# Optimization experiments

Hardware: AMD Instinct MI355X
Metric: run time of the kernel (lower is better)

## Reference

```python
import jax, jax.numpy as jnp
import numpy as np

EMBED = 256      # embedding_dim
HEADS = 4        # attn_heads
OUT = EMBED // HEADS  # out_channels per head = 64
R = 8            # n_relations = len(metapaths) + 1
N = 16384        # num_nodes
NEG_SLOPE = 0.2  # PyG GATv2 default leaky_relu slope


def setup_inputs() -> dict:
    key = jax.random.key(0)
    ks = jax.random.split(key, 16)
    s = 0.05
    inp = {"relation_embs": jax.random.normal(ks[0], (N, R, EMBED), jnp.float32)}
    # Two GATv2Conv layers: lin_l (src), lin_r (dst), att vector, output bias.
    for i in range(2):
        inp[f"Wl{i}"] = jax.random.normal(ks[1 + 6 * i], (EMBED, HEADS, OUT), jnp.float32) * s
        inp[f"bl{i}"] = jax.random.normal(ks[2 + 6 * i], (HEADS, OUT), jnp.float32) * s
        inp[f"Wr{i}"] = jax.random.normal(ks[3 + 6 * i], (EMBED, HEADS, OUT), jnp.float32) * s
        inp[f"br{i}"] = jax.random.normal(ks[4 + 6 * i], (HEADS, OUT), jnp.float32) * s
        inp[f"att{i}"] = jax.random.normal(ks[5 + 6 * i], (HEADS, OUT), jnp.float32) * s
        inp[f"bias{i}"] = jax.random.normal(ks[6 + 6 * i], (HEADS * OUT,), jnp.float32) * s
    return inp


def reference(relation_embs, Wl0, bl0, Wr0, br0, att0, bias0,
              Wl1, bl1, Wr1, br1, att1, bias1):
    # Each node owns a fully-connected graph over its R relation embeddings
    # (all rows nonzero under randn fill), so the PyG gather/softmax/scatter
    # collapses to dense [N, R_dst, R_src] attention.
    h = jax.nn.relu(relation_embs)                                  # [N,R,D]

    # ---- GATv2 layer 0: full FC edges (every src -> every dst) ----
    xl = jnp.einsum('nrd,dhc->nrhc', h, Wl0) + bl0                  # src feats [N,R,H,C]
    xr = jnp.einsum('nrd,dhc->nrhc', h, Wr0) + br0                  # dst feats [N,R,H,C]
    e = jax.nn.leaky_relu(xr[:, :, None] + xl[:, None], NEG_SLOPE)  # [N,Ri,Rj,H,C]
    logits = jnp.einsum('nijhc,hc->nijh', e, att0)                  # [N,Ri,Rj,H]
    alpha = jax.nn.softmax(logits, axis=2)                          # softmax over src j
    h = jnp.einsum('nijh,njhc->nihc', alpha, xl)                    # [N,R,H,C]
    h = h.reshape(N, R, HEADS * OUT) + bias0
    h = jax.nn.relu(h)

    # ---- GATv2 layer 1 (last): only edges into the self node (nid == R-1) ----
    xl = jnp.einsum('nrd,dhc->nrhc', h, Wl1) + bl1                  # src feats [N,R,H,C]
    xr_self = jnp.einsum('nd,dhc->nhc', h[:, -1], Wr1) + br1        # dst = self [N,H,C]
    e = jax.nn.leaky_relu(xr_self[:, None] + xl, NEG_SLOPE)         # [N,R,H,C]
    logits = jnp.einsum('nrhc,hc->nrh', e, att1)                    # [N,R,H]
    alpha = jax.nn.softmax(logits, axis=1)                          # softmax over src r
    out = jnp.einsum('nrh,nrhc->nhc', alpha, xl).reshape(N, HEADS * OUT) + bias1
    node_embs = jax.nn.relu(out)                                    # [N, D]

    # betas: last-layer attention into the self node, detached (SparseTensor.to_dense().detach())
    betas = jax.lax.stop_gradient(alpha)                            # [N,R,H]
    return node_embs, betas
```

## Files before the change

### kernel.cpp

```cpp
#include <hip/hip_runtime.h>


#define NNODES 16384
#define NB 8
#define MR 64

typedef _Float16 f16x8 __attribute__((ext_vector_type(8)));
typedef _Float16 f16x4 __attribute__((ext_vector_type(4)));
typedef _Float16 f16x2 __attribute__((ext_vector_type(2)));
typedef float f32x4 __attribute__((ext_vector_type(4)));

#if __has_builtin(__builtin_amdgcn_fdot2)
#define FDOT2(a, b, c) __builtin_amdgcn_fdot2((a), (b), (c), false)
#else
#define FDOT2(a, b, c) ((c) + (float)(a)[0] * (float)(b)[0] + (float)(a)[1] * (float)(b)[1])
#endif

__device__ __forceinline__ f16x2 pk2(float a, float b) {
    return __builtin_bit_cast(f16x2, __builtin_amdgcn_cvt_pkrtz(a, b));
}

__device__ __forceinline__ f16x2 leaky2(f16x2 t) {
#if __has_builtin(__builtin_elementwise_max)
    return __builtin_elementwise_max(t, t * (f16x2){(_Float16)0.2f, (_Float16)0.2f});
#else
    const unsigned u = __builtin_bit_cast(unsigned, t) & 0x7FFF7FFFu;
    const f16x2 at = __builtin_bit_cast(f16x2, u);
    return t * (f16x2){(_Float16)0.6f, (_Float16)0.6f} +
           at * (f16x2){(_Float16)0.4f, (_Float16)0.4f};
#endif
}
__device__ __forceinline__ f16x2 relu2(f16x2 t) {
#if __has_builtin(__builtin_elementwise_max)
    return __builtin_elementwise_max(t, (f16x2){(_Float16)0.f, (_Float16)0.f});
#else
    const unsigned u = __builtin_bit_cast(unsigned, t) & 0x7FFF7FFFu;
    const f16x2 at = __builtin_bit_cast(f16x2, u);
    return (t + at) * (f16x2){(_Float16)0.5f, (_Float16)0.5f};
#endif
}

__device__ __forceinline__ int swz(int row, int chunk) {
    return row * 256 + ((chunk ^ (row & 7)) << 3);
}

__global__ void prep_weights(const float* __restrict__ Wl0, const float* __restrict__ Wr0,
                             const float* __restrict__ Wl1, const float* __restrict__ Wr1,
                             _Float16* __restrict__ wt) {
    __shared__ float tile[64 * 68];
    const int t  = threadIdx.x;
    const int m  = blockIdx.x >> 4;
    const int kt = (blockIdx.x >> 2) & 3;
    const int nt = blockIdx.x & 3;
    const float* src = (m == 0 ? Wl0 : m == 1 ? Wr0 : m == 2 ? Wl1 : Wr1) + kt * 64 * 256;
    #pragma unroll
    for (int i = 0; i < 4; ++i) {
        const int idx = i * 256 + t;
        const int kk  = idx >> 4;
        const int nn  = (idx & 15) * 4;
        const float4 v = *(const float4*)&src[kk * 256 + nt * 64 + nn];
        tile[kk * 68 + nn + 0] = v.x;
        tile[kk * 68 + nn + 1] = v.y;
        tile[kk * 68 + nn + 2] = v.z;
        tile[kk * 68 + nn + 3] = v.w;
    }
    __syncthreads();
    const int n  = t >> 2;
    const int ks = (t & 3) * 16;
    f16x8 o0, o1;
    #pragma unroll
    for (int e = 0; e < 8; ++e) o0[e] = (_Float16)tile[(ks + e) * 68 + n];
    #pragma unroll
    for (int e = 0; e < 8; ++e) o1[e] = (_Float16)tile[(ks + 8 + e) * 68 + n];
    _Float16* dst = &wt[(size_t)(m * 256 + nt * 64 + n) * 256 + kt * 64 + ks];
    *(f16x8*)dst = o0;
    *(f16x8*)(dst + 8) = o1;
}

__launch_bounds__(512, 4)
__global__ void gat_fused(const float* __restrict__ x,
                          const float* __restrict__ bl0, const float* __restrict__ br0,
                          const float* __restrict__ att0, const float* __restrict__ bias0,
                          const float* __restrict__ bl1, const float* __restrict__ br1,
                          const float* __restrict__ att1, const float* __restrict__ bias1,
                          const _Float16* __restrict__ wt,
                          float* __restrict__ out) {
    __shared__ _Float16 bufA[MR * 256];
    __shared__ _Float16 bufB[MR * 256];
    __shared__ float attbuf[2304];
    __shared__ _Float16 attH[768];

    const int tid  = threadIdx.x;
    const int bg   = blockIdx.x;
    const int lane = tid & 63;
    const int wv   = tid >> 6;
    const int lr   = lane & 15;
    const int lq   = lane >> 4;

    {
        const float4* src = (const float4*)(x + (size_t)bg * (MR * 256));
        #pragma unroll
        for (int it = 0; it < 4; ++it) {
            const int g   = it * 512 + tid;
            const int row = g >> 5;
            const int c   = g & 31;
            const float4 v0 = src[2 * g];
            const float4 v1 = src[2 * g + 1];
            f16x8 s;
            s[0] = (_Float16)fmaxf(v0.x, 0.f); s[1] = (_Float16)fmaxf(v0.y, 0.f);
            s[2] = (_Float16)fmaxf(v0.z, 0.f); s[3] = (_Float16)fmaxf(v0.w, 0.f);
            s[4] = (_Float16)fmaxf(v1.x, 0.f); s[5] = (_Float16)fmaxf(v1.y, 0.f);
            s[6] = (_Float16)fmaxf(v1.z, 0.f); s[7] = (_Float16)fmaxf(v1.w, 0.f);
            *(f16x8*)&bufA[swz(row, c)] = s;
        }
        if (tid < 256) {
            attH[tid]       = (_Float16)att0[tid];
            attH[512 + tid] = (_Float16)bias0[tid];
        } else {
            attH[tid]       = (_Float16)att1[tid - 256];
        }
    }
    __syncthreads();

    {
        f32x4 acc[4][4];
        #pragma unroll
        for (int m = 0; m < 4; ++m)
            #pragma unroll
            for (int n = 0; n < 4; ++n)
                acc[m][n] = f32x4{0.f, 0.f, 0.f, 0.f};
        #pragma unroll
        for (int kt = 0; kt < 8; ++kt) {
            f16x8 a[4], b[4];
            #pragma unroll
            for (int m = 0; m < 4; ++m)
                a[m] = *(const f16x8*)&bufA[swz(m * 16 + lr, kt * 4 + lq)];
            const int koff = kt * 32 + lq * 8;
            #pragma unroll
            for (int n = 0; n < 4; ++n)
                b[n] = *(const f16x8*)&wt[(size_t)(wv * 64 + n * 16 + lr) * 256 + koff];
            #pragma unroll
            for (int m = 0; m < 4; ++m)
                #pragma unroll
                for (int n = 0; n < 4; ++n)
                    acc[m][n] = __builtin_amdgcn_mfma_f32_16x16x32_f16(a[m], b[n], acc[m][n], 0, 0, 0);
        }
        __syncthreads();
        _Float16* dstbuf = (wv < 4) ? bufB : bufA;
        const float* bv = (wv < 4) ? bl0 : br0;
        #pragma unroll
        for (int n = 0; n < 4; ++n) {
            const int cl   = (wv & 3) * 64 + n * 16 + lr;
            const float bias = bv[cl];
            const int ch   = cl >> 3, ce = cl & 7;
            #pragma unroll
            for (int m = 0; m < 4; ++m)
                #pragma unroll
                for (int r = 0; r < 4; ++r) {
                    const int row = m * 16 + lq * 4 + r;
                    dstbuf[swz(row, ch) + ce] = (_Float16)(acc[m][n][r] + bias);
                }
        }
    }
    __syncthreads();

    {
        const int n  = tid >> 6;
        const int i  = (tid >> 3) & 7;
        const int h  = (tid >> 1) & 3;
        const int jh = tid & 1;
        const int rowR = n * 8 + i;
        f16x2 xr2[32];
        #pragma unroll
        for (int cc = 0; cc < 8; ++cc) {
            const int c3 = (cc + 2 * h) & 7;
            const f16x8 v = *(const f16x8*)&bufA[swz(rowR, h * 8 + c3)];
            xr2[cc * 4 + 0] = f16x2{v[0], v[1]};
            xr2[cc * 4 + 1] = f16x2{v[2], v[3]};
            xr2[cc * 4 + 2] = f16x2{v[4], v[5]};
            xr2[cc * 4 + 3] = f16x2{v[6], v[7]};
        }
        f16x8 lbuf[2][4];
        f16x8 abuf[2];
        {
            const int c3 = (2 * h) & 7;
            abuf[0] = *(const f16x8*)&attH[h * 64 + c3 * 8];
            #pragma unroll
            for (int jj = 0; jj < 4; ++jj)
                lbuf[0][jj] = *(const f16x8*)&bufB[swz(n * 8 + jh * 4 + jj, h * 8 + c3)];
        }
        float lg[4] = {0.f, 0.f, 0.f, 0.f};
        #pragma unroll
        for (int cc = 0; cc < 8; ++cc) {
            const int cur = cc & 1, nxt = cur ^ 1;
            if (cc < 7) {
                const int c3n = (cc + 1 + 2 * h) & 7;
                abuf[nxt] = *(const f16x8*)&attH[h * 64 + c3n * 8];
                #pragma unroll
                for (int jj = 0; jj < 4; ++jj)
                    lbuf[nxt][jj] = *(const f16x8*)&bufB[swz(n * 8 + jh * 4 + jj, h * 8 + c3n)];
            }
            const f16x8 a8 = abuf[cur];
            const f16x2 a2[4] = {{a8[0], a8[1]}, {a8[2], a8[3]}, {a8[4], a8[5]}, {a8[6], a8[7]}};
            #pragma unroll
            for (int jj = 0; jj < 4; ++jj) {
                const f16x8 l8 = lbuf[cur][jj];
                const f16x2 l2[4] = {{l8[0], l8[1]}, {l8[2], l8[3]}, {l8[4], l8[5]}, {l8[6], l8[7]}};
                #pragma unroll
                for (int p = 0; p < 4; ++p) {
                    const f16x2 t = leaky2(xr2[cc * 4 + p] + l2[p]);
                    lg[jj] = FDOT2(t, a2[p], lg[jj]);
                }
            }
        }
        float mx = fmaxf(fmaxf(lg[0], lg[1]), fmaxf(lg[2], lg[3]));
        mx = fmaxf(mx, __shfl_xor(mx, 1));
        float ex[4], ssum = 0.f;
        #pragma unroll
        for (int jj = 0; jj < 4; ++jj) { ex[jj] = __expf(lg[jj] - mx); ssum += ex[jj]; }
        const float tot = ssum + __shfl_xor(ssum, 1);
        const float inv = 1.f / tot;
        #pragma unroll
        for (int jj = 0; jj < 4; ++jj)
            attbuf[((n * 8 + i) * 4 + h) * 8 + jh * 4 + jj] = ex[jj] * inv;
    }
    __syncthreads();

    {
        const int row  = tid >> 3;
        const int sub  = tid & 7;
        const int h    = sub >> 1;
        const int half = sub & 1;
        const int nn   = row >> 3;
        const int cb   = h * 8 + half * 4;
        _Float16 ahv[8];
        #pragma unroll
        for (int j = 0; j < 8; ++j) ahv[j] = (_Float16)attbuf[(row * 4 + h) * 8 + j];
        f16x2 acc2[16];
        #pragma unroll
        for (int p = 0; p < 16; ++p) acc2[p] = (f16x2){(_Float16)0.f, (_Float16)0.f};
        f16x8 vbuf[2][4];
        #pragma unroll
        for (int cc = 0; cc < 4; ++cc)
            vbuf[0][cc] = *(const f16x8*)&bufB[swz(nn * 8, cb + ((cc + h) & 3))];
        #pragma unroll
        for (int j = 0; j < 8; ++j) {
            const int cur = j & 1, nxt = cur ^ 1;
            if (j < 7) {
                #pragma unroll
                for (int cc = 0; cc < 4; ++cc)
                    vbuf[nxt][cc] = *(const f16x8*)&bufB[swz(nn * 8 + j + 1, cb + ((cc + h) & 3))];
            }
            const f16x2 a2 = {ahv[j], ahv[j]};
            #pragma unroll
            for (int cc = 0; cc < 4; ++cc) {
                const f16x8 v = vbuf[cur][cc];
                acc2[cc * 4 + 0] += f16x2{v[0], v[1]} * a2;
                acc2[cc * 4 + 1] += f16x2{v[2], v[3]} * a2;
                acc2[cc * 4 + 2] += f16x2{v[4], v[5]} * a2;
                acc2[cc * 4 + 3] += f16x2{v[6], v[7]} * a2;
            }
        }
        #pragma unroll
        for (int cc = 0; cc < 4; ++cc) {
            const int c = cb + ((cc + h) & 3);
            const f16x8 b8 = *(const f16x8*)&attH[512 + c * 8];
            f16x8 s;
            #pragma unroll
            for (int p = 0; p < 4; ++p) {
                const f16x2 r = relu2(acc2[cc * 4 + p] + f16x2{b8[2 * p], b8[2 * p + 1]});
                s[2 * p]     = r[0];
                s[2 * p + 1] = r[1];
            }
            *(f16x8*)&bufA[swz(row, c)] = s;
        }
    }
    __syncthreads();

    {
        f32x4 accl[4][2], accr[2];
        #pragma unroll
        for (int m = 0; m < 4; ++m)
            #pragma unroll
            for (int n = 0; n < 2; ++n)
                accl[m][n] = f32x4{0.f, 0.f, 0.f, 0.f};
        #pragma unroll
        for (int n = 0; n < 2; ++n) accr[n] = f32x4{0.f, 0.f, 0.f, 0.f};
        const _Float16* W1l = wt + 512 * 256;
        const _Float16* W1r = wt + 768 * 256;
        const int rowS = (lr & 7) * 8 + 7;
        #pragma unroll
        for (int kt = 0; kt < 8; ++kt) {
            const int koff = kt * 32 + lq * 8;
            f16x8 a[4], as, bl[2], br[2];
            #pragma unroll
            for (int m = 0; m < 4; ++m)
                a[m] = *(const f16x8*)&bufA[swz(m * 16 + lr, kt * 4 + lq)];
            as = *(const f16x8*)&bufA[swz(rowS, kt * 4 + lq)];
            #pragma unroll
            for (int n = 0; n < 2; ++n) {
                bl[n] = *(const f16x8*)&W1l[(size_t)(wv * 32 + n * 16 + lr) * 256 + koff];
                br[n] = *(const f16x8*)&W1r[(size_t)(wv * 32 + n * 16 + lr) * 256 + koff];
            }
            #pragma unroll
            for (int m = 0; m < 4; ++m)
                #pragma unroll
                for (int n = 0; n < 2; ++n)
                    accl[m][n] = __builtin_amdgcn_mfma_f32_16x16x32_f16(a[m], bl[n], accl[m][n], 0, 0, 0);
            #pragma unroll
            for (int n = 0; n < 2; ++n)
                accr[n] = __builtin_amdgcn_mfma_f32_16x16x32_f16(as, br[n], accr[n], 0, 0, 0);
        }
        #pragma unroll
        for (int n = 0; n < 2; ++n) {
            const int col = wv * 32 + n * 16 + lr;
            const float b1 = bl1[col], b2 = br1[col];
            const int ch = col >> 3, ce = col & 7;
            #pragma unroll
            for (int m = 0; m < 4; ++m)
                #pragma unroll
                for (int r = 0; r < 4; ++r) {
                    const int row = m * 16 + lq * 4 + r;
                    bufB[swz(row, ch) + ce] = (_Float16)(accl[m][n][r] + b1);
                }
            if (lq < 2) {
                #pragma unroll
                for (int r = 0; r < 4; ++r) {
                    const int node = lq * 4 + r;
                    attbuf[node * 256 + col] = accr[n][r] + b2;
                }
            }
        }
    }
    __syncthreads();

    {
        const int n  = tid >> 5;
        const int rr = (tid >> 2) & 7;
        const int h  = tid & 3;
        float lg = 0.f;
        if (tid < 256) {
            const int rowj = n * 8 + rr;
            float4 xbuf0[2], xbuf1[2];
            f16x8 lbuf[2], abuf[2];
            {
                const int c = h * 8 + ((2 * h) & 7);
                xbuf0[0] = *(const float4*)&attbuf[n * 256 + c * 8];
                xbuf1[0] = *(const float4*)&attbuf[n * 256 + c * 8 + 4];
                lbuf[0]  = *(const f16x8*)&bufB[swz(rowj, c)];
                abuf[0]  = *(const f16x8*)&attH[256 + c * 8];
            }
            #pragma unroll
            for (int cc = 0; cc < 8; ++cc) {
                const int cur = cc & 1, nxt = cur ^ 1;
                if (cc < 7) {
                    const int cn = h * 8 + ((cc + 1 + 2 * h) & 7);
                    xbuf0[nxt] = *(const float4*)&attbuf[n * 256 + cn * 8];
                    xbuf1[nxt] = *(const float4*)&attbuf[n * 256 + cn * 8 + 4];
                    lbuf[nxt]  = *(const f16x8*)&bufB[swz(rowj, cn)];
                    abuf[nxt]  = *(const f16x8*)&attH[256 + cn * 8];
                }
                const float4 r0 = xbuf0[cur], r1 = xbuf1[cur];
                const f16x2 x2[4] = {pk2(r0.x, r0.y), pk2(r0.z, r0.w),
                                     pk2(r1.x, r1.y), pk2(r1.z, r1.w)};
                const f16x8 l8 = lbuf[cur];
                const f16x2 l2[4] = {{l8[0], l8[1]}, {l8[2], l8[3]}, {l8[4], l8[5]}, {l8[6], l8[7]}};
                const f16x8 a8 = abuf[cur];
                const f16x2 a2[4] = {{a8[0], a8[1]}, {a8[2], a8[3]}, {a8[4], a8[5]}, {a8[6], a8[7]}};
                #pragma unroll
                for (int p = 0; p < 4; ++p) {
                    const f16x2 t = leaky2(x2[p] + l2[p]);
                    lg = FDOT2(t, a2[p], lg);
                }
            }
        }
        __syncthreads();
        if (tid < 256) attbuf[2048 + tid] = lg;
        __syncthreads();
        if (tid < 256) {
            float M = -1e30f;
            float l[8];
            #pragma unroll
            for (int j = 0; j < 8; ++j) {
                l[j] = attbuf[2048 + n * 32 + j * 4 + h];
                M = fmaxf(M, l[j]);
            }
            float S = 0.f;
            #pragma unroll
            for (int j = 0; j < 8; ++j) S += __expf(l[j] - M);
            const float a = __expf(lg - M) / S;
            attbuf[tid] = a;
            out[(size_t)NNODES * 256 + (size_t)(bg * NB + n) * 32 + rr * 4 + h] = a;
        }
    }
    __syncthreads();

    {
        const int n  = tid >> 6;
        const int q  = tid & 63;
        const int c0 = q * 4;
        const int h  = q >> 4;
        f16x4 v[8];
        float a[8];
        #pragma unroll
        for (int r = 0; r < 8; ++r) {
            v[r] = *(const f16x4*)&bufB[swz(n * 8 + r, q >> 1) + (q & 1) * 4];
            a[r] = attbuf[n * 32 + r * 4 + h];
        }
        float o0 = 0.f, o1 = 0.f, o2 = 0.f, o3 = 0.f;
        #pragma unroll
        for (int r = 0; r < 8; ++r) {
            o0 = fmaf((float)v[r][0], a[r], o0);
            o1 = fmaf((float)v[r][1], a[r], o1);
            o2 = fmaf((float)v[r][2], a[r], o2);
            o3 = fmaf((float)v[r][3], a[r], o3);
        }
        float4 res;
        res.x = fmaxf(o0 + bias1[c0 + 0], 0.f);
        res.y = fmaxf(o1 + bias1[c0 + 1], 0.f);
        res.z = fmaxf(o2 + bias1[c0 + 2], 0.f);
        res.w = fmaxf(o3 + bias1[c0 + 3], 0.f);
        *(float4*)&out[(size_t)(bg * NB + n) * 256 + c0] = res;
    }
}

extern "C" void kernel_launch(void* const* d_in, const int* in_sizes, int n_in,
                              void* d_out, int out_size, void* d_ws, size_t ws_size,
                              hipStream_t stream) {
    const float* x     = (const float*)d_in[0];
    const float* Wl0   = (const float*)d_in[1];
    const float* bl0   = (const float*)d_in[2];
    const float* Wr0   = (const float*)d_in[3];
    const float* br0   = (const float*)d_in[4];
    const float* att0  = (const float*)d_in[5];
    const float* bias0 = (const float*)d_in[6];
    const float* Wl1   = (const float*)d_in[7];
    const float* bl1   = (const float*)d_in[8];
    const float* Wr1   = (const float*)d_in[9];
    const float* br1   = (const float*)d_in[10];
    const float* att1  = (const float*)d_in[11];
    const float* bias1 = (const float*)d_in[12];
    _Float16* wt = (_Float16*)d_ws;
    float* out = (float*)d_out;

    prep_weights<<<64, 256, 0, stream>>>(Wl0, Wr0, Wl1, Wr1, wt);
    gat_fused<<<NNODES / NB, 512, 0, stream>>>(x, bl0, br0, att0, bias0,
                                               bl1, br1, att1, bias1, wt, out);
}
```

Baseline: 350.7 us.

## Halve per-block node tile to 4 nodes with 256 threads and fp16 LDS buffers

Shrinks each block from 8 nodes/512 threads to 4 nodes/256 threads, remapping the MFMA warp tiling so each wave covers more output columns and fewer rows. The shared float attbuf is replaced by smaller fp16 buffers for attention weights and self-destination features, plus separate logit and alpha arrays, which removes a barrier and the float-to-half packing in layer 1. The aim is lower LDS per block so more blocks fit per CU, and better latency hiding. The cost is that each block now re-reads the full weight matrices for half as many nodes, doubling global and L2 weight traffic.

```diff
diff --git a/kernel.cpp b/kernel.cpp
--- a/kernel.cpp
+++ b/kernel.cpp
@@ -2,8 +2,8 @@
 
 
 #define NNODES 16384
-#define NB 8
-#define MR 64
+#define NB 4
+#define MR 32
 
 typedef _Float16 f16x8 __attribute__((ext_vector_type(8)));
 typedef _Float16 f16x4 __attribute__((ext_vector_type(4)));
@@ -15,10 +15,6 @@
 #else
 #define FDOT2(a, b, c) ((c) + (float)(a)[0] * (float)(b)[0] + (float)(a)[1] * (float)(b)[1])
 #endif
-
-__device__ __forceinline__ f16x2 pk2(float a, float b) {
-    return __builtin_bit_cast(f16x2, __builtin_amdgcn_cvt_pkrtz(a, b));
-}
 
 __device__ __forceinline__ f16x2 leaky2(f16x2 t) {
 #if __has_builtin(__builtin_elementwise_max)
@@ -77,7 +73,7 @@
     *(f16x8*)(dst + 8) = o1;
 }
 
-__launch_bounds__(512, 4)
+__launch_bounds__(256, 4)
 __global__ void gat_fused(const float* __restrict__ x,
                           const float* __restrict__ bl0, const float* __restrict__ br0,
                           const float* __restrict__ att0, const float* __restrict__ bias0,
@@ -87,7 +83,10 @@
                           float* __restrict__ out) {
     __shared__ _Float16 bufA[MR * 256];
     __shared__ _Float16 bufB[MR * 256];
-    __shared__ float attbuf[2304];
+    __shared__ _Float16 aw[MR * 4 * 8];
+    __shared__ _Float16 xrsH[NB * 256];
+    __shared__ float lgs[NB * 32];
+    __shared__ float al1[NB * 32];
     __shared__ _Float16 attH[768];
 
     const int tid  = threadIdx.x;
@@ -101,7 +100,7 @@
         const float4* src = (const float4*)(x + (size_t)bg * (MR * 256));
         #pragma unroll
         for (int it = 0; it < 4; ++it) {
-            const int g   = it * 512 + tid;
+            const int g   = it * 256 + tid;
             const int row = g >> 5;
             const int c   = g & 31;
             const float4 v0 = src[2 * g];
@@ -113,48 +112,45 @@
             s[6] = (_Float16)fmaxf(v1.z, 0.f); s[7] = (_Float16)fmaxf(v1.w, 0.f);
             *(f16x8*)&bufA[swz(row, c)] = s;
         }
-        if (tid < 256) {
-            attH[tid]       = (_Float16)att0[tid];
-            attH[512 + tid] = (_Float16)bias0[tid];
-        } else {
-            attH[tid]       = (_Float16)att1[tid - 256];
-        }
-    }
-    __syncthreads();
-
-    {
-        f32x4 acc[4][4];
-        #pragma unroll
-        for (int m = 0; m < 4; ++m)
-            #pragma unroll
-            for (int n = 0; n < 4; ++n)
+        attH[tid]       = (_Float16)att0[tid];
+        attH[256 + tid] = (_Float16)att1[tid];
+        attH[512 + tid] = (_Float16)bias0[tid];
+    }
+    __syncthreads();
+
+    {
+        f32x4 acc[2][8];
+        #pragma unroll
+        for (int m = 0; m < 2; ++m)
+            #pragma unroll
+            for (int n = 0; n < 8; ++n)
                 acc[m][n] = f32x4{0.f, 0.f, 0.f, 0.f};
         #pragma unroll
         for (int kt = 0; kt < 8; ++kt) {
-            f16x8 a[4], b[4];
-            #pragma unroll
-            for (int m = 0; m < 4; ++m)
+            f16x8 a[2], b[8];
+            #pragma unroll
+            for (int m = 0; m < 2; ++m)
                 a[m] = *(const f16x8*)&bufA[swz(m * 16 + lr, kt * 4 + lq)];
             const int koff = kt * 32 + lq * 8;
             #pragma unroll
-            for (int n = 0; n < 4; ++n)
-                b[n] = *(const f16x8*)&wt[(size_t)(wv * 64 + n * 16 + lr) * 256 + koff];
-            #pragma unroll
-            for (int m = 0; m < 4; ++m)
-                #pragma unroll
-                for (int n = 0; n < 4; ++n)
+            for (int n = 0; n < 8; ++n)
+                b[n] = *(const f16x8*)&wt[(size_t)(wv * 128 + n * 16 + lr) * 256 + koff];
+            #pragma unroll
+            for (int m = 0; m < 2; ++m)
+                #pragma unroll
+                for (int n = 0; n < 8; ++n)
                     acc[m][n] = __builtin_amdgcn_mfma_f32_16x16x32_f16(a[m], b[n], acc[m][n], 0, 0, 0);
         }
         __syncthreads();
-        _Float16* dstbuf = (wv < 4) ? bufB : bufA;
-        const float* bv = (wv < 4) ? bl0 : br0;
-        #pragma unroll
-        for (int n = 0; n < 4; ++n) {
-            const int cl   = (wv & 3) * 64 + n * 16 + lr;
+        _Float16* dstbuf = (wv < 2) ? bufB : bufA;
+        const float* bv = (wv < 2) ? bl0 : br0;
+        #pragma unroll
+        for (int n = 0; n < 8; ++n) {
+            const int cl   = (wv & 1) * 128 + n * 16 + lr;
             const float bias = bv[cl];
             const int ch   = cl >> 3, ce = cl & 7;
             #pragma unroll
-            for (int m = 0; m < 4; ++m)
+            for (int m = 0; m < 2; ++m)
                 #pragma unroll
                 for (int r = 0; r < 4; ++r) {
                     const int row = m * 16 + lq * 4 + r;
@@ -220,9 +216,10 @@
         for (int jj = 0; jj < 4; ++jj) { ex[jj] = __expf(lg[jj] - mx); ssum += ex[jj]; }
         const float tot = ssum + __shfl_xor(ssum, 1);
         const float inv = 1.f / tot;
-        #pragma unroll
-        for (int jj = 0; jj < 4; ++jj)
-            attbuf[((n * 8 + i) * 4 + h) * 8 + jh * 4 + jj] = ex[jj] * inv;
+        f16x4 w;
+        #pragma unroll
+        for (int jj = 0; jj < 4; ++jj) w[jj] = (_Float16)(ex[jj] * inv);
+        *(f16x4*)&aw[((n * 8 + i) * 4 + h) * 8 + jh * 4] = w;
     }
     __syncthreads();
 
@@ -233,9 +230,7 @@
         const int half = sub & 1;
         const int nn   = row >> 3;
         const int cb   = h * 8 + half * 4;
-        _Float16 ahv[8];
-        #pragma unroll
-        for (int j = 0; j < 8; ++j) ahv[j] = (_Float16)attbuf[(row * 4 + h) * 8 + j];
+        const f16x8 ah8 = *(const f16x8*)&aw[(row * 4 + h) * 8];
         f16x2 acc2[16];
         #pragma unroll
         for (int p = 0; p < 16; ++p) acc2[p] = (f16x2){(_Float16)0.f, (_Float16)0.f};
@@ -251,7 +246,7 @@
                 for (int cc = 0; cc < 4; ++cc)
                     vbuf[nxt][cc] = *(const f16x8*)&bufB[swz(nn * 8 + j + 1, cb + ((cc + h) & 3))];
             }
-            const f16x2 a2 = {ahv[j], ahv[j]};
+            const f16x2 a2 = {ah8[j], ah8[j]};
             #pragma unroll
             for (int cc = 0; cc < 4; ++cc) {
                 const f16x8 v = vbuf[cur][cc];
@@ -278,57 +273,55 @@
     __syncthreads();
 
     {
-        f32x4 accl[4][2], accr[2];
-        #pragma unroll
-        for (int m = 0; m < 4; ++m)
-            #pragma unroll
-            for (int n = 0; n < 2; ++n)
+        f32x4 accl[2][4], accr[4];
+        #pragma unroll
+        for (int m = 0; m < 2; ++m)
+            #pragma unroll
+            for (int n = 0; n < 4; ++n)
                 accl[m][n] = f32x4{0.f, 0.f, 0.f, 0.f};
         #pragma unroll
-        for (int n = 0; n < 2; ++n) accr[n] = f32x4{0.f, 0.f, 0.f, 0.f};
+        for (int n = 0; n < 4; ++n) accr[n] = f32x4{0.f, 0.f, 0.f, 0.f};
         const _Float16* W1l = wt + 512 * 256;
         const _Float16* W1r = wt + 768 * 256;
-        const int rowS = (lr & 7) * 8 + 7;
+        const int rowS = (lr & 3) * 8 + 7;
         #pragma unroll
         for (int kt = 0; kt < 8; ++kt) {
             const int koff = kt * 32 + lq * 8;
-            f16x8 a[4], as, bl[2], br[2];
-            #pragma unroll
-            for (int m = 0; m < 4; ++m)
+            f16x8 a[2], as, bl[4], br[4];
+            #pragma unroll
+            for (int m = 0; m < 2; ++m)
                 a[m] = *(const f16x8*)&bufA[swz(m * 16 + lr, kt * 4 + lq)];
             as = *(const f16x8*)&bufA[swz(rowS, kt * 4 + lq)];
             #pragma unroll
-            for (int n = 0; n < 2; ++n) {
-                bl[n] = *(const f16x8*)&W1l[(size_t)(wv * 32 + n * 16 + lr) * 256 + koff];
-                br[n] = *(const f16x8*)&W1r[(size_t)(wv * 32 + n * 16 + lr) * 256 + koff];
-            }
-            #pragma unroll
-            for (int m = 0; m < 4; ++m)
-                #pragma unroll
-                for (int n = 0; n < 2; ++n)
+            for (int n = 0; n < 4; ++n) {
+                bl[n] = *(const f16x8*)&W1l[(size_t)(wv * 64 + n * 16 + lr) * 256 + koff];
+                br[n] = *(const f16x8*)&W1r[(size_t)(wv * 64 + n * 16 + lr) * 256 + koff];
+            }
+            #pragma unroll
+            for (int m = 0; m < 2; ++m)
+                #pragma unroll
+                for (int n = 0; n < 4; ++n)
                     accl[m][n] = __builtin_amdgcn_mfma_f32_16x16x32_f16(a[m], bl[n], accl[m][n], 0, 0, 0);
             #pragma unroll
-            for (int n = 0; n < 2; ++n)
+            for (int n = 0; n < 4; ++n)
                 accr[n] = __builtin_amdgcn_mfma_f32_16x16x32_f16(as, br[n], accr[n], 0, 0, 0);
         }
         #pragma unroll
-        for (int n = 0; n < 2; ++n) {
-            const int col = wv * 32 + n * 16 + lr;
+        for (int n = 0; n < 4; ++n) {
+            const int col = wv * 64 + n * 16 + lr;
             const float b1 = bl1[col], b2 = br1[col];
             const int ch = col >> 3, ce = col & 7;
             #pragma unroll
-            for (int m = 0; m < 4; ++m)
+            for (int m = 0; m < 2; ++m)
                 #pragma unroll
                 for (int r = 0; r < 4; ++r) {
                     const int row = m * 16 + lq * 4 + r;
                     bufB[swz(row, ch) + ce] = (_Float16)(accl[m][n][r] + b1);
                 }
-            if (lq < 2) {
-                #pragma unroll
-                for (int r = 0; r < 4; ++r) {
-                    const int node = lq * 4 + r;
-                    attbuf[node * 256 + col] = accr[n][r] + b2;
-                }
+            if (lq == 0) {
+                #pragma unroll
+                for (int r = 0; r < 4; ++r)
+                    xrsH[r * 256 + col] = (_Float16)(accr[n][r] + b2);
             }
         }
     }
@@ -339,57 +332,52 @@
         const int rr = (tid >> 2) & 7;
         const int h  = tid & 3;
         float lg = 0.f;
-        if (tid < 256) {
+        if (tid < 128) {
             const int rowj = n * 8 + rr;
-            float4 xbuf0[2], xbuf1[2];
-            f16x8 lbuf[2], abuf[2];
+            f16x8 xbuf[2], lbuf[2], abuf[2];
             {
                 const int c = h * 8 + ((2 * h) & 7);
-                xbuf0[0] = *(const float4*)&attbuf[n * 256 + c * 8];
-                xbuf1[0] = *(const float4*)&attbuf[n * 256 + c * 8 + 4];
-                lbuf[0]  = *(const f16x8*)&bufB[swz(rowj, c)];
-                abuf[0]  = *(const f16x8*)&attH[256 + c * 8];
+                xbuf[0] = *(const f16x8*)&xrsH[n * 256 + c * 8];
+                lbuf[0] = *(const f16x8*)&bufB[swz(rowj, c)];
+                abuf[0] = *(const f16x8*)&attH[256 + c * 8];
             }
             #pragma unroll
             for (int cc = 0; cc < 8; ++cc) {
                 const int cur = cc & 1, nxt = cur ^ 1;
                 if (cc < 7) {
                     const int cn = h * 8 + ((cc + 1 + 2 * h) & 7);
-                    xbuf0[nxt] = *(const float4*)&attbuf[n * 256 + cn * 8];
-                    xbuf1[nxt] = *(const float4*)&attbuf[n * 256 + cn * 8 + 4];
-                    lbuf[nxt]  = *(const f16x8*)&bufB[swz(rowj, cn)];
-                    abuf[nxt]  = *(const f16x8*)&attH[256 + cn * 8];
+                    xbuf[nxt] = *(const f16x8*)&xrsH[n * 256 + cn * 8];
+                    lbuf[nxt] = *(const f16x8*)&bufB[swz(rowj, cn)];
+                    abuf[nxt] = *(const f16x8*)&attH[256 + cn * 8];
                 }
-                const float4 r0 = xbuf0[cur], r1 = xbuf1[cur];
-                const f16x2 x2[4] = {pk2(r0.x, r0.y), pk2(r0.z, r0.w),
-                                     pk2(r1.x, r1.y), pk2(r1.z, r1.w)};
+                const f16x8 x8 = xbuf[cur];
                 const f16x8 l8 = lbuf[cur];
-                const f16x2 l2[4] = {{l8[0], l8[1]}, {l8[2], l8[3]}, {l8[4], l8[5]}, {l8[6], l8[7]}};
                 const f16x8 a8 = abuf[cur];
-                const f16x2 a2[4] = {{a8[0], a8[1]}, {a8[2], a8[3]}, {a8[4], a8[5]}, {a8[6], a8[7]}};
                 #pragma unroll
                 for (int p = 0; p < 4; ++p) {
-                    const f16x2 t = leaky2(x2[p] + l2[p]);
-                    lg = FDOT2(t, a2[p], lg);
+                    const f16x2 xp = {x8[2 * p], x8[2 * p + 1]};
+                    const f16x2 lp = {l8[2 * p], l8[2 * p + 1]};
+                    const f16x2 ap = {a8[2 * p], a8[2 * p + 1]};
+                    const f16x2 t = leaky2(xp + lp);
+                    lg = FDOT2(t, ap, lg);
                 }
             }
+            lgs[tid] = lg;
         }
         __syncthreads();
-        if (tid < 256) attbuf[2048 + tid] = lg;
-        __syncthreads();
-        if (tid < 256) {
+        if (tid < 128) {
             float M = -1e30f;
             float l[8];
             #pragma unroll
             for (int j = 0; j < 8; ++j) {
-                l[j] = attbuf[2048 + n * 32 + j * 4 + h];
+                l[j] = lgs[n * 32 + j * 4 + h];
                 M = fmaxf(M, l[j]);
             }
             float S = 0.f;
             #pragma unroll
             for (int j = 0; j < 8; ++j) S += __expf(l[j] - M);
             const float a = __expf(lg - M) / S;
-            attbuf[tid] = a;
+            al1[tid] = a;
             out[(size_t)NNODES * 256 + (size_t)(bg * NB + n) * 32 + rr * 4 + h] = a;
         }
     }
@@ -405,7 +393,7 @@
         #pragma unroll
         for (int r = 0; r < 8; ++r) {
             v[r] = *(const f16x4*)&bufB[swz(n * 8 + r, q >> 1) + (q & 1) * 4];
-            a[r] = attbuf[n * 32 + r * 4 + h];
+            a[r] = al1[n * 32 + r * 4 + h];
         }
         float o0 = 0.f, o1 = 0.f, o2 = 0.f, o3 = 0.f;
         #pragma unroll
@@ -444,6 +432,6 @@
     float* out = (float*)d_out;
 
     prep_weights<<<64, 256, 0, stream>>>(Wl0, Wr0, Wl1, Wr1, wt);
-    gat_fused<<<NNODES / NB, 512, 0, stream>>>(x, bl0, br0, att0, bias0,
+    gat_fused<<<NNODES / NB, 256, 0, stream>>>(x, bl0, br0, att0, bias0,
                                                bl1, br1, att1, bias1, wt, out);
 }
```

Result: slower. 432.2 us (+23.2%).

## Split layer-0 projection GEMM into separate kernel with fp16 workspace intermediate

Applied to the files above, without the earlier changes.

Splits the fused kernel in two. A standalone GEMM kernel over 128-row tiles computes the layer-0 src/dst projections and writes them as fp16 into a workspace buffer. A second kernel reads that buffer and does the attention, the layer-1 GEMM and the output. This gives the first GEMM larger tiles and better weight reuse, at the cost of an extra global round trip of about 128MB (written, then read back) and a larger workspace requirement. If the workspace is too small, it falls back to the original fused kernel.

```diff
diff --git a/kernel.cpp b/kernel.cpp
--- a/kernel.cpp
+++ b/kernel.cpp
@@ -42,6 +42,9 @@
 
 __device__ __forceinline__ int swz(int row, int chunk) {
     return row * 256 + ((chunk ^ (row & 7)) << 3);
+}
+__device__ __forceinline__ int cswz(int row, int col) {
+    return row * 128 + (((col >> 3) ^ (row & 7)) << 3) + (col & 7);
 }
 
 __global__ void prep_weights(const float* __restrict__ Wl0, const float* __restrict__ Wr0,
@@ -78,6 +81,389 @@
 }
 
 __launch_bounds__(512, 4)
+__global__ void gemm0(const float* __restrict__ x,
+                      const float* __restrict__ bl0, const float* __restrict__ br0,
+                      const _Float16* __restrict__ wt,
+                      _Float16* __restrict__ X1) {
+    __shared__ _Float16 A[128 * 256];
+    const int bid = blockIdx.x;
+    const int mb = bid >> 2, nb = bid & 3;
+    const int row0 = mb * 128;
+    const int tid = threadIdx.x;
+    const int lane = tid & 63;
+    const int wv = tid >> 6;
+    const int lr = lane & 15;
+    const int lq = lane >> 4;
+    const int wr = wv >> 1;
+    const int wc = wv & 1;
+
+    {
+        const float4* src = (const float4*)(x + (size_t)row0 * 256);
+        #pragma unroll
+        for (int it = 0; it < 8; ++it) {
+            const int g = it * 512 + tid;
+            const int row = g >> 5, c = g & 31;
+            const float4 v0 = src[2 * g];
+            const float4 v1 = src[2 * g + 1];
+            f16x8 s;
+            s[0] = (_Float16)fmaxf(v0.x, 0.f); s[1] = (_Float16)fmaxf(v0.y, 0.f);
+            s[2] = (_Float16)fmaxf(v0.z, 0.f); s[3] = (_Float16)fmaxf(v0.w, 0.f);
+            s[4] = (_Float16)fmaxf(v1.x, 0.f); s[5] = (_Float16)fmaxf(v1.y, 0.f);
+            s[6] = (_Float16)fmaxf(v1.z, 0.f); s[7] = (_Float16)fmaxf(v1.w, 0.f);
+            *(f16x8*)&A[swz(row, c)] = s;
+        }
+    }
+    __syncthreads();
+
+    f32x4 acc[2][4];
+    #pragma unroll
+    for (int m = 0; m < 2; ++m)
+        #pragma unroll
+        for (int n = 0; n < 4; ++n)
+            acc[m][n] = f32x4{0.f, 0.f, 0.f, 0.f};
+    #pragma unroll
+    for (int kt = 0; kt < 8; ++kt) {
+        const int koff = kt * 32 + lq * 8;
+        f16x8 a[2], b[4];
+        #pragma unroll
+        for (int m = 0; m < 2; ++m)
+            a[m] = *(const f16x8*)&A[swz(wr * 32 + m * 16 + lr, kt * 4 + lq)];
+        #pragma unroll
+        for (int n = 0; n < 4; ++n)
+            b[n] = *(const f16x8*)&wt[(size_t)(nb * 128 + wc * 64 + n * 16 + lr) * 256 + koff];
+        #pragma unroll
+        for (int m = 0; m < 2; ++m)
+            #pragma unroll
+            for (int n = 0; n < 4; ++n)
+                acc[m][n] = __builtin_amdgcn_mfma_f32_16x16x32_f16(a[m], b[n], acc[m][n], 0, 0, 0);
+    }
+    __syncthreads();
+
+    _Float16* Cl = A;
+    #pragma unroll
+    for (int n = 0; n < 4; ++n) {
+        const int col  = wc * 64 + n * 16 + lr;
+        const int gcol = nb * 128 + col;
+        const float bias = (gcol < 256) ? bl0[gcol] : br0[gcol - 256];
+        #pragma unroll
+        for (int m = 0; m < 2; ++m)
+            #pragma unroll
+            for (int r = 0; r < 4; ++r) {
+                const int row = wr * 32 + m * 16 + lq * 4 + r;
+                Cl[cswz(row, col)] = (_Float16)(acc[m][n][r] + bias);
+            }
+    }
+    __syncthreads();
+
+    #pragma unroll
+    for (int it = 0; it < 4; ++it) {
+        const int g = it * 512 + tid;
+        const int row = g >> 4, ch = g & 15;
+        const f16x8 v = *(const f16x8*)&Cl[row * 128 + ((ch ^ (row & 7)) << 3)];
+        *(f16x8*)&X1[(size_t)(row0 + row) * 512 + nb * 128 + ch * 8] = v;
+    }
+}
+
+__launch_bounds__(512, 4)
+__global__ void gat_attn(const float* __restrict__ att0, const float* __restrict__ bias0,
+                         const float* __restrict__ bl1, const float* __restrict__ br1,
+                         const float* __restrict__ att1, const float* __restrict__ bias1,
+                         const _Float16* __restrict__ wt,
+                         const _Float16* __restrict__ X1,
+                         float* __restrict__ out) {
+    __shared__ _Float16 bufA[MR * 256];
+    __shared__ _Float16 bufB[MR * 256];
+    __shared__ float attbuf[2304];
+    __shared__ _Float16 attH[768];
+
+    const int tid  = threadIdx.x;
+    const int bg   = blockIdx.x;
+    const int lane = tid & 63;
+    const int wv   = tid >> 6;
+    const int lr   = lane & 15;
+    const int lq   = lane >> 4;
+
+    {
+        const _Float16* src = X1 + (size_t)bg * 64 * 512;
+        #pragma unroll
+        for (int it = 0; it < 4; ++it) {
+            const int g = it * 512 + tid;
+            const int row = g >> 5, c = g & 31;
+            const f16x8 vl = *(const f16x8*)&src[(size_t)row * 512 + c * 8];
+            const f16x8 vr = *(const f16x8*)&src[(size_t)row * 512 + 256 + c * 8];
+            *(f16x8*)&bufB[swz(row, c)] = vl;
+            *(f16x8*)&bufA[swz(row, c)] = vr;
+        }
+        if (tid < 256) {
+            attH[tid]       = (_Float16)att0[tid];
+            attH[512 + tid] = (_Float16)bias0[tid];
+        } else {
+            attH[tid]       = (_Float16)att1[tid - 256];
+        }
+    }
+    __syncthreads();
+
+    {
+        const int n  = tid >> 6;
+        const int i  = (tid >> 3) & 7;
+        const int h  = (tid >> 1) & 3;
+        const int jh = tid & 1;
+        const int rowR = n * 8 + i;
+        f16x2 xr2[32];
+        #pragma unroll
+        for (int cc = 0; cc < 8; ++cc) {
+            const int c3 = (cc + 2 * h) & 7;
+            const f16x8 v = *(const f16x8*)&bufA[swz(rowR, h * 8 + c3)];
+            xr2[cc * 4 + 0] = f16x2{v[0], v[1]};
+            xr2[cc * 4 + 1] = f16x2{v[2], v[3]};
+            xr2[cc * 4 + 2] = f16x2{v[4], v[5]};
+            xr2[cc * 4 + 3] = f16x2{v[6], v[7]};
+        }
+        f16x8 lbuf[2][4];
+        f16x8 abuf[2];
+        {
+            const int c3 = (2 * h) & 7;
+            abuf[0] = *(const f16x8*)&attH[h * 64 + c3 * 8];
+            #pragma unroll
+            for (int jj = 0; jj < 4; ++jj)
+                lbuf[0][jj] = *(const f16x8*)&bufB[swz(n * 8 + jh * 4 + jj, h * 8 + c3)];
+        }
+        float lg[4] = {0.f, 0.f, 0.f, 0.f};
+        #pragma unroll
+        for (int cc = 0; cc < 8; ++cc) {
+            const int cur = cc & 1, nxt = cur ^ 1;
+            if (cc < 7) {
+                const int c3n = (cc + 1 + 2 * h) & 7;
+                abuf[nxt] = *(const f16x8*)&attH[h * 64 + c3n * 8];
+                #pragma unroll
+                for (int jj = 0; jj < 4; ++jj)
+                    lbuf[nxt][jj] = *(const f16x8*)&bufB[swz(n * 8 + jh * 4 + jj, h * 8 + c3n)];
+            }
+            const f16x8 a8 = abuf[cur];
+            const f16x2 a2[4] = {{a8[0], a8[1]}, {a8[2], a8[3]}, {a8[4], a8[5]}, {a8[6], a8[7]}};
+            #pragma unroll
+            for (int jj = 0; jj < 4; ++jj) {
+                const f16x8 l8 = lbuf[cur][jj];
+                const f16x2 l2[4] = {{l8[0], l8[1]}, {l8[2], l8[3]}, {l8[4], l8[5]}, {l8[6], l8[7]}};
+                #pragma unroll
+                for (int p = 0; p < 4; ++p) {
+                    const f16x2 t = leaky2(xr2[cc * 4 + p] + l2[p]);
+                    lg[jj] = FDOT2(t, a2[p], lg[jj]);
+                }
+            }
+        }
+        float mx = fmaxf(fmaxf(lg[0], lg[1]), fmaxf(lg[2], lg[3]));
+        mx = fmaxf(mx, __shfl_xor(mx, 1));
+        float ex[4], ssum = 0.f;
+        #pragma unroll
+        for (int jj = 0; jj < 4; ++jj) { ex[jj] = __expf(lg[jj] - mx); ssum += ex[jj]; }
+        const float tot = ssum + __shfl_xor(ssum, 1);
+        const float inv = 1.f / tot;
+        #pragma unroll
+        for (int jj = 0; jj < 4; ++jj)
+            attbuf[((n * 8 + i) * 4 + h) * 8 + jh * 4 + jj] = ex[jj] * inv;
+    }
+    __syncthreads();
+
+    {
+        const int row  = tid >> 3;
+        const int sub  = tid & 7;
+        const int h    = sub >> 1;
+        const int half = sub & 1;
+        const int nn   = row >> 3;
+        const int cb   = h * 8 + half * 4;
+        _Float16 ahv[8];
+        #pragma unroll
+        for (int j = 0; j < 8; ++j) ahv[j] = (_Float16)attbuf[(row * 4 + h) * 8 + j];
+        f16x2 acc2[16];
+        #pragma unroll
+        for (int p = 0; p < 16; ++p) acc2[p] = (f16x2){(_Float16)0.f, (_Float16)0.f};
+        f16x8 vbuf[2][4];
+        #pragma unroll
+        for (int cc = 0; cc < 4; ++cc)
+            vbuf[0][cc] = *(const f16x8*)&bufB[swz(nn * 8, cb + ((cc + h) & 3))];
+        #pragma unroll
+        for (int j = 0; j < 8; ++j) {
+            const int cur = j & 1, nxt = cur ^ 1;
+            if (j < 7) {
+                #pragma unroll
+                for (int cc = 0; cc < 4; ++cc)
+                    vbuf[nxt][cc] = *(const f16x8*)&bufB[swz(nn * 8 + j + 1, cb + ((cc + h) & 3))];
+            }
+            const f16x2 a2 = {ahv[j], ahv[j]};
+            #pragma unroll
+            for (int cc = 0; cc < 4; ++cc) {
+                const f16x8 v = vbuf[cur][cc];
+                acc2[cc * 4 + 0] += f16x2{v[0], v[1]} * a2;
+                acc2[cc * 4 + 1] += f16x2{v[2], v[3]} * a2;
+                acc2[cc * 4 + 2] += f16x2{v[4], v[5]} * a2;
+                acc2[cc * 4 + 3] += f16x2{v[6], v[7]} * a2;
+            }
+        }
+        #pragma unroll
+        for (int cc = 0; cc < 4; ++cc) {
+            const int c = cb + ((cc + h) & 3);
+            const f16x8 b8 = *(const f16x8*)&attH[512 + c * 8];
+            f16x8 s;
+            #pragma unroll
+            for (int p = 0; p < 4; ++p) {
+                const f16x2 r = relu2(acc2[cc * 4 + p] + f16x2{b8[2 * p], b8[2 * p + 1]});
+                s[2 * p]     = r[0];
+                s[2 * p + 1] = r[1];
+            }
+            *(f16x8*)&bufA[swz(row, c)] = s;
+        }
+    }
+    __syncthreads();
+
+    {
+        f32x4 accl[4][2], accr[2];
+        #pragma unroll
+        for (int m = 0; m < 4; ++m)
+            #pragma unroll
+            for (int n = 0; n < 2; ++n)
+                accl[m][n] = f32x4{0.f, 0.f, 0.f, 0.f};
+        #pragma unroll
+        for (int n = 0; n < 2; ++n) accr[n] = f32x4{0.f, 0.f, 0.f, 0.f};
+        const _Float16* W1l = wt + 512 * 256;
+        const _Float16* W1r = wt + 768 * 256;
+        const int rowS = (lr & 7) * 8 + 7;
+        #pragma unroll
+        for (int kt = 0; kt < 8; ++kt) {
+            const int koff = kt * 32 + lq * 8;
+            f16x8 a[4], as, bl[2], br[2];
+            #pragma unroll
+            for (int m = 0; m < 4; ++m)
+                a[m] = *(const f16x8*)&bufA[swz(m * 16 + lr, kt * 4 + lq)];
+            as = *(const f16x8*)&bufA[swz(rowS, kt * 4 + lq)];
+            #pragma unroll
+            for (int n = 0; n < 2; ++n) {
+                bl[n] = *(const f16x8*)&W1l[(size_t)(wv * 32 + n * 16 + lr) * 256 + koff];
+                br[n] = *(const f16x8*)&W1r[(size_t)(wv * 32 + n * 16 + lr) * 256 + koff];
+            }
+            #pragma unroll
+            for (int m = 0; m < 4; ++m)
+                #pragma unroll
+                for (int n = 0; n < 2; ++n)
+                    accl[m][n] = __builtin_amdgcn_mfma_f32_16x16x32_f16(a[m], bl[n], accl[m][n], 0, 0, 0);
+            #pragma unroll
+            for (int n = 0; n < 2; ++n)
+                accr[n] = __builtin_amdgcn_mfma_f32_16x16x32_f16(as, br[n], accr[n], 0, 0, 0);
+        }
+        #pragma unroll
+        for (int n = 0; n < 2; ++n) {
+            const int col = wv * 32 + n * 16 + lr;
+            const float b1 = bl1[col], b2 = br1[col];
+            const int ch = col >> 3, ce = col & 7;
+            #pragma unroll
+            for (int m = 0; m < 4; ++m)
+                #pragma unroll
+                for (int r = 0; r < 4; ++r) {
+                    const int row = m * 16 + lq * 4 + r;
+                    bufB[swz(row, ch) + ce] = (_Float16)(accl[m][n][r] + b1);
+                }
+            if (lq < 2) {
+                #pragma unroll
+                for (int r = 0; r < 4; ++r) {
+                    const int node = lq * 4 + r;
+                    attbuf[node * 256 + col] = accr[n][r] + b2;
+                }
+            }
+        }
+    }
+    __syncthreads();
+
+    {
+        const int n  = tid >> 5;
+        const int rr = (tid >> 2) & 7;
+        const int h  = tid & 3;
+        float lg = 0.f;
+        if (tid < 256) {
+            const int rowj = n * 8 + rr;
+            float4 xbuf0[2], xbuf1[2];
+            f16x8 lbuf[2], abuf[2];
+            {
+                const int c = h * 8 + ((2 * h) & 7);
+                xbuf0[0] = *(const float4*)&attbuf[n * 256 + c * 8];
+                xbuf1[0] = *(const float4*)&attbuf[n * 256 + c * 8 + 4];
+                lbuf[0]  = *(const f16x8*)&bufB[swz(rowj, c)];
+                abuf[0]  = *(const f16x8*)&attH[256 + c * 8];
+            }
+            #pragma unroll
+            for (int cc = 0; cc < 8; ++cc) {
+                const int cur = cc & 1, nxt = cur ^ 1;
+                if (cc < 7) {
+                    const int cn = h * 8 + ((cc + 1 + 2 * h) & 7);
+                    xbuf0[nxt] = *(const float4*)&attbuf[n * 256 + cn * 8];
+                    xbuf1[nxt] = *(const float4*)&attbuf[n * 256 + cn * 8 + 4];
+                    lbuf[nxt]  = *(const f16x8*)&bufB[swz(rowj, cn)];
+                    abuf[nxt]  = *(const f16x8*)&attH[256 + cn * 8];
+                }
+                const float4 r0 = xbuf0[cur], r1 = xbuf1[cur];
+                const f16x2 x2[4] = {pk2(r0.x, r0.y), pk2(r0.z, r0.w),
+                                     pk2(r1.x, r1.y), pk2(r1.z, r1.w)};
+                const f16x8 l8 = lbuf[cur];
+                const f16x2 l2[4] = {{l8[0], l8[1]}, {l8[2], l8[3]}, {l8[4], l8[5]}, {l8[6], l8[7]}};
+                const f16x8 a8 = abuf[cur];
+                const f16x2 a2[4] = {{a8[0], a8[1]}, {a8[2], a8[3]}, {a8[4], a8[5]}, {a8[6], a8[7]}};
+                #pragma unroll
+                for (int p = 0; p < 4; ++p) {
+                    const f16x2 t = leaky2(x2[p] + l2[p]);
+                    lg = FDOT2(t, a2[p], lg);
+                }
+            }
+        }
+        __syncthreads();
+        if (tid < 256) attbuf[2048 + tid] = lg;
+        __syncthreads();
+        if (tid < 256) {
+            float M = -1e30f;
+            float l[8];
+            #pragma unroll
+            for (int j = 0; j < 8; ++j) {
+                l[j] = attbuf[2048 + n * 32 + j * 4 + h];
+                M = fmaxf(M, l[j]);
+            }
+            float S = 0.f;
+            #pragma unroll
+            for (int j = 0; j < 8; ++j) S += __expf(l[j] - M);
+            const float a = __expf(lg - M) / S;
+            attbuf[tid] = a;
+            out[(size_t)NNODES * 256 + (size_t)(bg * NB + n) * 32 + rr * 4 + h] = a;
+        }
+    }
+    __syncthreads();
+
+    {
+        const int n  = tid >> 6;
+        const int q  = tid & 63;
+        const int c0 = q * 4;
+        const int h  = q >> 4;
+        f16x4 v[8];
+        float a[8];
+        #pragma unroll
+        for (int r = 0; r < 8; ++r) {
+            v[r] = *(const f16x4*)&bufB[swz(n * 8 + r, q >> 1) + (q & 1) * 4];
+            a[r] = attbuf[n * 32 + r * 4 + h];
+        }
+        float o0 = 0.f, o1 = 0.f, o2 = 0.f, o3 = 0.f;
+        #pragma unroll
+        for (int r = 0; r < 8; ++r) {
+            o0 = fmaf((float)v[r][0], a[r], o0);
+            o1 = fmaf((float)v[r][1], a[r], o1);
+            o2 = fmaf((float)v[r][2], a[r], o2);
+            o3 = fmaf((float)v[r][3], a[r], o3);
+        }
+        float4 res;
+        res.x = fmaxf(o0 + bias1[c0 + 0], 0.f);
+        res.y = fmaxf(o1 + bias1[c0 + 1], 0.f);
+        res.z = fmaxf(o2 + bias1[c0 + 2], 0.f);
+        res.w = fmaxf(o3 + bias1[c0 + 3], 0.f);
+        *(float4*)&out[(size_t)(bg * NB + n) * 256 + c0] = res;
+    }
+}
+
+__launch_bounds__(512, 4)
 __global__ void gat_fused(const float* __restrict__ x,
                           const float* __restrict__ bl0, const float* __restrict__ br0,
                           const float* __restrict__ att0, const float* __restrict__ bias0,
@@ -444,6 +830,16 @@
     float* out = (float*)d_out;
 
     prep_weights<<<64, 256, 0, stream>>>(Wl0, Wr0, Wl1, Wr1, wt);
-    gat_fused<<<NNODES / NB, 512, 0, stream>>>(x, bl0, br0, att0, bias0,
-                                               bl1, br1, att1, bias1, wt, out);
-}
+
+    const size_t X1_off  = 524288;
+    const size_t X1_size = (size_t)131072 * 512 * 2;
+    if (ws_size >= X1_off + X1_size) {
+        _Float16* X1 = (_Float16*)((char*)d_ws + X1_off);
+        gemm0<<<4096, 512, 0, stream>>>(x, bl0, br0, wt, X1);
+        gat_attn<<<NNODES / NB, 512, 0, stream>>>(att0, bias0, bl1, br1,
+                                                  att1, bias1, wt, X1, out);
+    } else {
+        gat_fused<<<NNODES / NB, 512, 0, stream>>>(x, bl0, br0, att0, bias0,
+                                                   bl1, br1, att1, bias1, wt, out);
+    }
+}
```

Result: slower. 443.2 us (+26.4%).
